# Optimization experiments

Measured on AMD Instinct MI355X. Metric: run time of the kernel, lower is better.

Reference implementation:

```python
import jax, jax.numpy as jnp
import numpy as np
from jax import lax

KERNEL = 3
EPS = 0.01


def _box_sum(x, k):
    # sum over kxk window, stride 1, SAME-style explicit padding of k//2
    pad = k // 2
    return lax.reduce_window(
        x, 0.0, lax.add,
        window_dimensions=(1, 1, k, k),
        window_strides=(1, 1, 1, 1),
        padding=((0, 0), (0, 0), (pad, pad), (pad, pad)),
    )


def _box_counts(h, w, k, dtype):
    # number of valid (non-padded) elements in each window (count_include_pad=False)
    ones = jnp.ones((1, 1, h, w), dtype=dtype)
    return _box_sum(ones, k)


def _blur(x, counts, k):
    return _box_sum(x, k) / counts


def setup_inputs() -> dict:
    key = jax.random.key(0)
    k1, k2 = jax.random.split(key)
    shape = (8, 16, 512, 512)
    inp = jax.random.normal(k1, shape, dtype=jnp.float32)
    guide = jax.random.normal(k2, shape, dtype=jnp.float32)
    return {"input": inp, "guide": guide}


def reference(input, guide):
    I, p = input, guide
    B, C, H, W = I.shape
    counts = _box_counts(H, W, KERNEL, I.dtype)  # [1,1,H,W]

    mean_I = _blur(I, counts, KERNEL)
    mean_p = _blur(p, counts, KERNEL)
    mean_II = _blur(I * I, counts, KERNEL)
    mean_Ip = _blur(I * p, counts, KERNEL)

    var_I = mean_II - mean_I * mean_I
    cov_Ip = mean_Ip - mean_I * mean_p

    a = cov_Ip / (var_I + EPS)
    b = mean_p - a * mean_I

    mean_a = _blur(a, counts, KERNEL)
    mean_b = _blur(b, counts, KERNEL)

    return mean_a * I + mean_b
```

## Files before the change

kernel.cpp:

```cpp
#include <hip/hip_runtime.h>


constexpr int W  = 512;
constexpr int H  = 512;
constexpr int TW = 64;
constexpr int TH = 16;
constexpr int IW = TW + 4;
constexpr int IH = TH + 4;
constexpr int AW = TW + 2;
constexpr int AH = TH + 2;
constexpr float EPS = 0.01f;

__global__ __launch_bounds__(256) void guide_filter_kernel(
    const float* __restrict__ I, const float* __restrict__ P,
    float* __restrict__ O)
{
    __shared__ __align__(16) float2 sIP[IH][IW];
    __shared__ float2 sAB[AH][AW];

    const int tid = threadIdx.x;
    const int x0  = blockIdx.x * TW;
    const int y0  = blockIdx.y * TH;
    const size_t img_off = (size_t)blockIdx.z * (size_t)(W * H);
    const float* Ibase = I + img_off;
    const float* Pbase = P + img_off;
    float*       Obase = (float*)O + img_off;

    for (int t = tid; t < 34 * IH; t += 256) {
        const int row = t / 34;
        const int cp  = t - row * 34;
        const int gy  = y0 - 2 + row;
        const int gx  = x0 - 2 + 2 * cp;
        float i0 = 0.f, i1 = 0.f, p0 = 0.f, p1 = 0.f;
        if (gy >= 0 && gy < H) {
            const int g = gy * W + gx;
            if (gx >= 0 && gx + 1 < W) {
                const float2 vi = *(const float2*)(Ibase + g);
                const float2 vp = *(const float2*)(Pbase + g);
                i0 = vi.x; i1 = vi.y; p0 = vp.x; p1 = vp.y;
            } else {
                if (gx >= 0 && gx < W)         { i0 = Ibase[g];     p0 = Pbase[g]; }
                if (gx + 1 >= 0 && gx + 1 < W) { i1 = Ibase[g + 1]; p1 = Pbase[g + 1]; }
            }
        }
        *(float4*)&sIP[row][2 * cp] = make_float4(i0, p0, i1, p1);
    }
    __syncthreads();

    if (tid < 3 * AW) {
        const int strip = tid / AW;
        const int ax    = tid - strip * AW;
        const int ay0   = strip * 6;

        float wI[6], wP[6], wII[6], wIP[6];
        #pragma unroll
        for (int j = 0; j < 6; ++j) { wI[j] = wP[j] = wII[j] = wIP[j] = 0.f; }

        #pragma unroll
        for (int c = 0; c < 3; ++c) {
            float2 v[8];
            #pragma unroll
            for (int j = 0; j < 8; ++j) v[j] = sIP[ay0 + j][ax + c];
            float ii[8], ip[8];
            #pragma unroll
            for (int j = 0; j < 8; ++j) {
                ii[j] = v[j].x * v[j].x;
                ip[j] = v[j].x * v[j].y;
            }
            #pragma unroll
            for (int j = 0; j < 6; ++j) {
                wI[j]  += v[j].x  + v[j + 1].x  + v[j + 2].x;
                wP[j]  += v[j].y  + v[j + 1].y  + v[j + 2].y;
                wII[j] += ii[j]   + ii[j + 1]   + ii[j + 2];
                wIP[j] += ip[j]   + ip[j + 1]   + ip[j + 2];
            }
        }

        const int gx = x0 - 1 + ax;
        const bool xok = (gx >= 0) & (gx < W);
        const float cx = 3.f - (float)(gx == 0) - (float)(gx == W - 1);
        #pragma unroll
        for (int j = 0; j < 6; ++j) {
            const int ay = ay0 + j;
            const int gy = y0 - 1 + ay;
            float a = 0.f, b = 0.f;
            if (xok & (gy >= 0) & (gy < H)) {
                const float cy  = 3.f - (float)(gy == 0) - (float)(gy == H - 1);
                const float inv = __builtin_amdgcn_rcpf(cx * cy);
                const float mI   = wI[j] * inv;
                const float mP   = wP[j] * inv;
                const float varI = fmaf(-mI, mI, wII[j] * inv);
                const float cov  = fmaf(-mI, mP, wIP[j] * inv);
                a = cov * __builtin_amdgcn_rcpf(varI + EPS);
                b = fmaf(-a, mI, mP);
            }
            sAB[ay][ax] = make_float2(a, b);
        }
    }
    __syncthreads();

    {
        const int x  = tid & 63;
        const int r0 = (tid >> 6) * 4;
        float2 ab[6][3];
        #pragma unroll
        for (int j = 0; j < 6; ++j)
            #pragma unroll
            for (int c = 0; c < 3; ++c)
                ab[j][c] = sAB[r0 + j][x + c];

        float hA[6], hB[6];
        #pragma unroll
        for (int j = 0; j < 6; ++j) {
            hA[j] = ab[j][0].x + ab[j][1].x + ab[j][2].x;
            hB[j] = ab[j][0].y + ab[j][1].y + ab[j][2].y;
        }

        const int gx = x0 + x;
        const float cx = 3.f - (float)(gx == 0) - (float)(gx == W - 1);
        #pragma unroll
        for (int j = 0; j < 4; ++j) {
            const int gy = y0 + r0 + j;
            const float cy  = 3.f - (float)(gy == 0) - (float)(gy == H - 1);
            const float inv = __builtin_amdgcn_rcpf(cx * cy);
            const float ma  = (hA[j] + hA[j + 1] + hA[j + 2]) * inv;
            const float mb  = (hB[j] + hB[j + 1] + hB[j + 2]) * inv;
            const float Ic  = sIP[r0 + j + 2][x + 2].x;
            Obase[gy * W + gx] = fmaf(ma, Ic, mb);
        }
    }
}

extern "C" void kernel_launch(void* const* d_in, const int* in_sizes, int n_in,
                              void* d_out, int out_size, void* d_ws, size_t ws_size,
                              hipStream_t stream) {
    const float* I = (const float*)d_in[0];
    const float* P = (const float*)d_in[1];
    float*       O = (float*)d_out;
    const int images = in_sizes[0] / (W * H);
    dim3 grid(W / TW, H / TH, images);
    guide_filter_kernel<<<grid, dim3(256), 0, stream>>>(I, P, O);
}
```

Measured before the change: 332.2 us.

## Taller tiles, interior fast path, sliding-window 2-wide box sums with vector LDS

Doubles the tile height to 32 rows, which cuts the halo overhead per output. Each thread now computes two adjacent columns with a rolling 3-row window of horizontal partial sums, using float4 shared-memory reads and float2 global stores. A templated interior path skips boundary checks and uses a constant 1/9 divisor, and launch bounds request 4 blocks per CU. This reduces LDS traffic, redundant adds and branching, at the cost of more code, higher shared-memory use per block and only 231 of 256 threads active in the middle stage.

```diff
diff --git a/kernel.cpp b/kernel.cpp
--- a/kernel.cpp
+++ b/kernel.cpp
@@ -4,130 +4,173 @@
 constexpr int W  = 512;
 constexpr int H  = 512;
 constexpr int TW = 64;
-constexpr int TH = 16;
-constexpr int IW = TW + 4;
-constexpr int IH = TH + 4;
-constexpr int AW = TW + 2;
-constexpr int AH = TH + 2;
-constexpr float EPS = 0.01f;
+constexpr int TH = 32;
+constexpr int IPH = TH + 4;
+constexpr int IPW = TW + 4;
+constexpr int ABH = TH + 2;
+constexpr int ABW = TW + 2;
+constexpr float EPS  = 0.01f;
+constexpr float INV9 = 1.0f / 9.0f;
 
-__global__ __launch_bounds__(256) void guide_filter_kernel(
+template<bool INT>
+__device__ __forceinline__ void run_tile(
+    const float* __restrict__ Ibase, const float* __restrict__ Pbase,
+    float* __restrict__ Obase, int x0, int y0, int tid,
+    float2 (*sIP)[IPW], float2 (*sAB)[ABW])
+{
+    if (INT) {
+        #pragma unroll 2
+        for (int t = tid; t < 34 * IPH; t += 256) {
+            const int row = t / 34;
+            const int pc  = t - row * 34;
+            const int g   = (y0 - 2 + row) * W + (x0 - 2 + 2 * pc);
+            const float2 vi = *(const float2*)(Ibase + g);
+            const float2 vp = *(const float2*)(Pbase + g);
+            *(float4*)&sIP[row][2 * pc] = make_float4(vi.x, vp.x, vi.y, vp.y);
+        }
+    } else {
+        for (int t = tid; t < 34 * IPH; t += 256) {
+            const int row = t / 34;
+            const int pc  = t - row * 34;
+            const int gy  = y0 - 2 + row;
+            const int gx  = x0 - 2 + 2 * pc;
+            float i0 = 0.f, i1 = 0.f, q0 = 0.f, q1 = 0.f;
+            if (gy >= 0 && gy < H) {
+                const int g = gy * W + gx;
+                if (gx >= 0 && gx + 1 < W) {
+                    const float2 vi = *(const float2*)(Ibase + g);
+                    const float2 vp = *(const float2*)(Pbase + g);
+                    i0 = vi.x; i1 = vi.y; q0 = vp.x; q1 = vp.y;
+                } else {
+                    if ((unsigned)gx < (unsigned)W)       { i0 = Ibase[g];     q0 = Pbase[g]; }
+                    if ((unsigned)(gx + 1) < (unsigned)W) { i1 = Ibase[g + 1]; q1 = Pbase[g + 1]; }
+                }
+            }
+            *(float4*)&sIP[row][2 * pc] = make_float4(i0, q0, i1, q1);
+        }
+    }
+    __syncthreads();
+
+    if (tid < 231) {
+        const int p    = tid % 33;
+        const int s    = tid / 33;
+        const int row0 = 5 * s;
+
+        float hI[2][3], hP[2][3], hII[2][3], hIP[2][3];
+        #pragma unroll
+        for (int j = 0; j < 7; ++j) {
+            int rr = row0 + j; rr = rr > IPH - 1 ? IPH - 1 : rr;
+            const float4 c01 = *(const float4*)&sIP[rr][2 * p];
+            const float4 c23 = *(const float4*)&sIP[rr][2 * p + 2];
+            const float i0 = c01.x, q0 = c01.y, i1 = c01.z, q1 = c01.w;
+            const float i2 = c23.x, q2 = c23.y, i3 = c23.z, q3 = c23.w;
+            const int k = j % 3;
+            const float tI  = i1 + i2, tP = q1 + q2;
+            const float tII = fmaf(i1, i1, i2 * i2);
+            const float tIP = fmaf(i1, q1, i2 * q2);
+            hI[0][k]  = tI + i0;            hI[1][k]  = tI + i3;
+            hP[0][k]  = tP + q0;            hP[1][k]  = tP + q3;
+            hII[0][k] = fmaf(i0, i0, tII);  hII[1][k] = fmaf(i3, i3, tII);
+            hIP[0][k] = fmaf(i0, q0, tIP);  hIP[1][k] = fmaf(i3, q3, tIP);
+            if (j >= 2) {
+                const int ay = row0 + j - 2;
+                if (ay < ABH) {
+                    float ab[4];
+                    #pragma unroll
+                    for (int c = 0; c < 2; ++c) {
+                        const float wI  = hI[c][0]  + hI[c][1]  + hI[c][2];
+                        const float wP  = hP[c][0]  + hP[c][1]  + hP[c][2];
+                        const float wII = hII[c][0] + hII[c][1] + hII[c][2];
+                        const float wIP = hIP[c][0] + hIP[c][1] + hIP[c][2];
+                        float a = 0.f, b = 0.f;
+                        if (INT) {
+                            const float mI   = wI * INV9, mP = wP * INV9;
+                            const float varI = fmaf(-mI, mI, wII * INV9);
+                            const float cov  = fmaf(-mI, mP, wIP * INV9);
+                            a = cov * __builtin_amdgcn_rcpf(varI + EPS);
+                            b = fmaf(-a, mI, mP);
+                        } else {
+                            const int gx = x0 - 1 + 2 * p + c;
+                            const int gy = y0 - 1 + ay;
+                            if ((unsigned)gx < (unsigned)W && (unsigned)gy < (unsigned)H) {
+                                const float cx = 3.f - (float)(gx == 0) - (float)(gx == W - 1);
+                                const float cy = 3.f - (float)(gy == 0) - (float)(gy == H - 1);
+                                const float inv  = __builtin_amdgcn_rcpf(cx * cy);
+                                const float mI   = wI * inv, mP = wP * inv;
+                                const float varI = fmaf(-mI, mI, wII * inv);
+                                const float cov  = fmaf(-mI, mP, wIP * inv);
+                                a = cov * __builtin_amdgcn_rcpf(varI + EPS);
+                                b = fmaf(-a, mI, mP);
+                            }
+                        }
+                        ab[2 * c] = a; ab[2 * c + 1] = b;
+                    }
+                    *(float4*)&sAB[ay][2 * p] = make_float4(ab[0], ab[1], ab[2], ab[3]);
+                }
+            }
+        }
+    }
+    __syncthreads();
+
+    {
+        const int q   = tid & 31;
+        const int r   = tid >> 5;
+        const int ox0 = 2 * q;
+        const int oy0 = 4 * r;
+        float hA[2][3], hB[2][3];
+        #pragma unroll
+        for (int j = 0; j < 6; ++j) {
+            const float4 c01 = *(const float4*)&sAB[oy0 + j][ox0];
+            const float4 c23 = *(const float4*)&sAB[oy0 + j][ox0 + 2];
+            const float a0 = c01.x, b0 = c01.y, a1 = c01.z, b1 = c01.w;
+            const float a2 = c23.x, b2 = c23.y, a3 = c23.z, b3 = c23.w;
+            const int k = j % 3;
+            const float tA = a1 + a2, tB = b1 + b2;
+            hA[0][k] = tA + a0; hA[1][k] = tA + a3;
+            hB[0][k] = tB + b0; hB[1][k] = tB + b3;
+            if (j >= 2) {
+                const int oy = oy0 + j - 2;
+                const float4 ic = *(const float4*)&sIP[oy + 2][ox0 + 2];
+                float res[2];
+                #pragma unroll
+                for (int c = 0; c < 2; ++c) {
+                    const float sa = hA[c][0] + hA[c][1] + hA[c][2];
+                    const float sb = hB[c][0] + hB[c][1] + hB[c][2];
+                    float inv;
+                    if (INT) {
+                        inv = INV9;
+                    } else {
+                        const int gx = x0 + ox0 + c, gy = y0 + oy;
+                        const float cx = 3.f - (float)(gx == 0) - (float)(gx == W - 1);
+                        const float cy = 3.f - (float)(gy == 0) - (float)(gy == H - 1);
+                        inv = __builtin_amdgcn_rcpf(cx * cy);
+                    }
+                    const float Ic = (c == 0) ? ic.x : ic.z;
+                    res[c] = fmaf(sa * inv, Ic, sb * inv);
+                }
+                *(float2*)(Obase + (y0 + oy) * W + x0 + ox0) = make_float2(res[0], res[1]);
+            }
+        }
+    }
+}
+
+__global__ __launch_bounds__(256, 4) void guide_filter_kernel(
     const float* __restrict__ I, const float* __restrict__ P,
     float* __restrict__ O)
 {
-    __shared__ __align__(16) float2 sIP[IH][IW];
-    __shared__ float2 sAB[AH][AW];
+    __shared__ __align__(16) float2 sIP[IPH][IPW];
+    __shared__ __align__(16) float2 sAB[ABH][ABW];
 
     const int tid = threadIdx.x;
     const int x0  = blockIdx.x * TW;
     const int y0  = blockIdx.y * TH;
     const size_t img_off = (size_t)blockIdx.z * (size_t)(W * H);
-    const float* Ibase = I + img_off;
-    const float* Pbase = P + img_off;
-    float*       Obase = (float*)O + img_off;
-
-    for (int t = tid; t < 34 * IH; t += 256) {
-        const int row = t / 34;
-        const int cp  = t - row * 34;
-        const int gy  = y0 - 2 + row;
-        const int gx  = x0 - 2 + 2 * cp;
-        float i0 = 0.f, i1 = 0.f, p0 = 0.f, p1 = 0.f;
-        if (gy >= 0 && gy < H) {
-            const int g = gy * W + gx;
-            if (gx >= 0 && gx + 1 < W) {
-                const float2 vi = *(const float2*)(Ibase + g);
-                const float2 vp = *(const float2*)(Pbase + g);
-                i0 = vi.x; i1 = vi.y; p0 = vp.x; p1 = vp.y;
-            } else {
-                if (gx >= 0 && gx < W)         { i0 = Ibase[g];     p0 = Pbase[g]; }
-                if (gx + 1 >= 0 && gx + 1 < W) { i1 = Ibase[g + 1]; p1 = Pbase[g + 1]; }
-            }
-        }
-        *(float4*)&sIP[row][2 * cp] = make_float4(i0, p0, i1, p1);
-    }
-    __syncthreads();
-
-    if (tid < 3 * AW) {
-        const int strip = tid / AW;
-        const int ax    = tid - strip * AW;
-        const int ay0   = strip * 6;
-
-        float wI[6], wP[6], wII[6], wIP[6];
-        #pragma unroll
-        for (int j = 0; j < 6; ++j) { wI[j] = wP[j] = wII[j] = wIP[j] = 0.f; }
-
-        #pragma unroll
-        for (int c = 0; c < 3; ++c) {
-            float2 v[8];
-            #pragma unroll
-            for (int j = 0; j < 8; ++j) v[j] = sIP[ay0 + j][ax + c];
-            float ii[8], ip[8];
-            #pragma unroll
-            for (int j = 0; j < 8; ++j) {
-                ii[j] = v[j].x * v[j].x;
-                ip[j] = v[j].x * v[j].y;
-            }
-            #pragma unroll
-            for (int j = 0; j < 6; ++j) {
-                wI[j]  += v[j].x  + v[j + 1].x  + v[j + 2].x;
-                wP[j]  += v[j].y  + v[j + 1].y  + v[j + 2].y;
-                wII[j] += ii[j]   + ii[j + 1]   + ii[j + 2];
-                wIP[j] += ip[j]   + ip[j + 1]   + ip[j + 2];
-            }
-        }
-
-        const int gx = x0 - 1 + ax;
-        const bool xok = (gx >= 0) & (gx < W);
-        const float cx = 3.f - (float)(gx == 0) - (float)(gx == W - 1);
-        #pragma unroll
-        for (int j = 0; j < 6; ++j) {
-            const int ay = ay0 + j;
-            const int gy = y0 - 1 + ay;
-            float a = 0.f, b = 0.f;
-            if (xok & (gy >= 0) & (gy < H)) {
-                const float cy  = 3.f - (float)(gy == 0) - (float)(gy == H - 1);
-                const float inv = __builtin_amdgcn_rcpf(cx * cy);
-                const float mI   = wI[j] * inv;
-                const float mP   = wP[j] * inv;
-                const float varI = fmaf(-mI, mI, wII[j] * inv);
-                const float cov  = fmaf(-mI, mP, wIP[j] * inv);
-                a = cov * __builtin_amdgcn_rcpf(varI + EPS);
-                b = fmaf(-a, mI, mP);
-            }
-            sAB[ay][ax] = make_float2(a, b);
-        }
-    }
-    __syncthreads();
-
-    {
-        const int x  = tid & 63;
-        const int r0 = (tid >> 6) * 4;
-        float2 ab[6][3];
-        #pragma unroll
-        for (int j = 0; j < 6; ++j)
-            #pragma unroll
-            for (int c = 0; c < 3; ++c)
-                ab[j][c] = sAB[r0 + j][x + c];
-
-        float hA[6], hB[6];
-        #pragma unroll
-        for (int j = 0; j < 6; ++j) {
-            hA[j] = ab[j][0].x + ab[j][1].x + ab[j][2].x;
-            hB[j] = ab[j][0].y + ab[j][1].y + ab[j][2].y;
-        }
-
-        const int gx = x0 + x;
-        const float cx = 3.f - (float)(gx == 0) - (float)(gx == W - 1);
-        #pragma unroll
-        for (int j = 0; j < 4; ++j) {
-            const int gy = y0 + r0 + j;
-            const float cy  = 3.f - (float)(gy == 0) - (float)(gy == H - 1);
-            const float inv = __builtin_amdgcn_rcpf(cx * cy);
-            const float ma  = (hA[j] + hA[j + 1] + hA[j + 2]) * inv;
-            const float mb  = (hB[j] + hB[j + 1] + hB[j + 2]) * inv;
-            const float Ic  = sIP[r0 + j + 2][x + 2].x;
-            Obase[gy * W + gx] = fmaf(ma, Ic, mb);
-        }
+    const bool interior = (blockIdx.x > 0) & (blockIdx.x < gridDim.x - 1) &
+                          (blockIdx.y > 0) & (blockIdx.y < gridDim.y - 1);
+    if (interior) {
+        run_tile<true >(I + img_off, P + img_off, (float*)O + img_off, x0, y0, tid, sIP, sAB);
+    } else {
+        run_tile<false>(I + img_off, P + img_off, (float*)O + img_off, x0, y0, tid, sIP, sAB);
     }
 }
 
```

Measured after the change: 325.2 us. -2.1%, faster.
